# Kernel optimization log

Measured on AMD Instinct MI355X. Metric: run time of the kernel, lower is better.

The kernel has to match this reference:

```python
import jax, jax.numpy as jnp
import numpy as np

DIM = 1024
HIDDEN = 4096
NUM_EXPERTS = 8
TOP_K = 2
T = 8192


def setup_inputs() -> dict:
    key = jax.random.key(0)
    ks = jax.random.split(key, 5)
    scale = 0.02
    x = jax.random.normal(ks[0], (T, DIM), dtype=jnp.float32)
    gate_w = jax.random.normal(ks[1], (NUM_EXPERTS, DIM), dtype=jnp.float32) * scale  # Linear weight [out,in]
    w1 = jax.random.normal(ks[2], (NUM_EXPERTS, HIDDEN, DIM), dtype=jnp.float32) * scale
    w2 = jax.random.normal(ks[3], (NUM_EXPERTS, DIM, HIDDEN), dtype=jnp.float32) * scale
    w3 = jax.random.normal(ks[4], (NUM_EXPERTS, HIDDEN, DIM), dtype=jnp.float32) * scale
    return {"x": x, "gate_w": gate_w, "w1": w1, "w2": w2, "w3": w3}


def reference(x, gate_w, w1, w2, w3):
    # Router: softmax over all experts, take top-2, renormalize.
    logits = jnp.einsum('td,ed->te', x, gate_w)            # [T, E]
    probs = jax.nn.softmax(logits, axis=-1)
    topw, topi = jax.lax.top_k(probs, TOP_K)               # [T, 2]
    topw = topw / jnp.sum(topw, axis=-1, keepdims=True)
    out = jnp.zeros_like(x)
    num_experts = w1.shape[0]
    for e in range(num_experts):
        # combine weight for expert e per token (0 if not routed here)
        w_e = jnp.sum(jnp.where(topi == e, topw, 0.0), axis=-1)   # [T]
        h = jax.nn.silu(x @ w1[e].T) * (x @ w3[e].T)              # [T, HIDDEN]
        out = out + w_e[:, None] * (h @ w2[e].T)                  # [T, DIM]
    return out
```

## Files before the change

kernel.cpp:

```cpp
#include <hip/hip_runtime.h>
#include <hip/hip_bf16.h>
#include <cstdint>
#include <cstddef>

#define TK 8192
#define DIM 1024
#define HID 4096
#define NE 8

typedef __attribute__((ext_vector_type(8))) __bf16 bfrag;
typedef __attribute__((ext_vector_type(4))) float ffrag;

static __device__ __forceinline__ ushort f2bf(float f) {
    union { float f; uint32_t u; } v; v.f = f;
    uint32_t r = (v.u + 0x7fffu + ((v.u >> 16) & 1u)) >> 16;
    return (ushort)r;
}

static __device__ __forceinline__ uint4 pack8(float4 a, float4 b) {
    union { ushort u[8]; uint4 q; } pk;
    pk.u[0] = f2bf(a.x); pk.u[1] = f2bf(a.y); pk.u[2] = f2bf(a.z); pk.u[3] = f2bf(a.w);
    pk.u[4] = f2bf(b.x); pk.u[5] = f2bf(b.y); pk.u[6] = f2bf(b.z); pk.u[7] = f2bf(b.w);
    return pk.q;
}

static __device__ __forceinline__ void gld16(const ushort* g, ushort* l) {
    __builtin_amdgcn_global_load_lds(
        (const __attribute__((address_space(1))) unsigned int*)g,
        (__attribute__((address_space(3))) unsigned int*)l, 16, 0, 0);
}

#define BARRIER() asm volatile("s_barrier" ::: "memory")
#define WAITVM(N) asm volatile("s_waitcnt vmcnt(" #N ")" ::: "memory")

#define LDSIDX(r, kc) ((((r) >> 3) << 8) + ((kc) << 6) + (((r) & 7) << 3))
#define SLOT_R(s)  ((((s) >> 5) << 3) | ((s) & 7))
#define SLOT_KC(s) (((s) >> 3) & 3)

__global__ __launch_bounds__(256) void k_cvt(const float* __restrict__ src,
                                             ushort* __restrict__ dst, int n8) {
    int i = blockIdx.x * blockDim.x + threadIdx.x;
    if (i >= n8) return;
    const float4* p = (const float4*)src + (size_t)i * 2;
    ((uint4*)dst)[i] = pack8(p[0], p[1]);
}

__global__ __launch_bounds__(256) void k_router(const float* __restrict__ x,
                                                const float* __restrict__ gw,
                                                int* __restrict__ topi, float* __restrict__ topw) {
    int t = blockIdx.x * 4 + (threadIdx.x >> 6);
    int lane = threadIdx.x & 63;
    if (t >= TK) return;
    double acc[NE];
#pragma unroll
    for (int e = 0; e < NE; ++e) acc[e] = 0.0;
    const float* xr = x + (size_t)t * DIM;
    for (int k = lane; k < DIM; k += 64) {
        double xv = (double)xr[k];
#pragma unroll
        for (int e = 0; e < NE; ++e) acc[e] += xv * (double)gw[e * DIM + k];
    }
#pragma unroll
    for (int e = 0; e < NE; ++e) {
#pragma unroll
        for (int off = 32; off > 0; off >>= 1) acc[e] += __shfl_xor(acc[e], off);
    }
    if (lane == 0) {
        int i1 = 0;
#pragma unroll
        for (int e = 1; e < NE; ++e) if (acc[e] > acc[i1]) i1 = e;
        int i2 = (i1 == 0) ? 1 : 0;
#pragma unroll
        for (int e = 0; e < NE; ++e) if (e != i1 && acc[e] > acc[i2]) i2 = e;
        double w = 1.0 / (1.0 + exp(acc[i2] - acc[i1]));
        topi[t * 2 + 0] = i1; topi[t * 2 + 1] = i2;
        topw[t * 2 + 0] = (float)w; topw[t * 2 + 1] = (float)(1.0 - w);
    }
}

__global__ void k_count(const int* __restrict__ topi, int* __restrict__ counts) {
    int i = blockIdx.x * blockDim.x + threadIdx.x;
    if (i < 2 * TK) atomicAdd(&counts[topi[i]], 1);
}

__global__ void k_scan(const int* __restrict__ counts, int* __restrict__ offs,
                       int* __restrict__ cursor,
                       int* __restrict__ desc256, int* __restrict__ nd256,
                       int* __restrict__ desc128, int* __restrict__ nd128) {
    if (threadIdx.x == 0 && blockIdx.x == 0) {
        int s = 0, dA = 0, dB = 0;
        for (int e = 0; e < NE; ++e) {
            offs[e] = s; cursor[e] = s;
            int tA = (counts[e] + 255) >> 8;
            for (int t = 0; t < tA; ++t) desc256[dA++] = (e << 16) | t;
            int tB = (counts[e] + 127) >> 7;
            for (int t = 0; t < tB; ++t) desc128[dB++] = (e << 16) | t;
            s += counts[e];
        }
        offs[NE] = s;
        nd256[0] = dA; nd128[0] = dB;
    }
}

__global__ void k_scatter(const int* __restrict__ topi, const float* __restrict__ topw,
                          int* __restrict__ cursor, int* __restrict__ perm, float* __restrict__ pw) {
    int t = blockIdx.x * blockDim.x + threadIdx.x;
    if (t >= TK) return;
#pragma unroll
    for (int k = 0; k < 2; ++k) {
        int e = topi[t * 2 + k];
        int pos = atomicAdd(&cursor[e], 1);
        perm[pos] = t; pw[pos] = topw[t * 2 + k];
    }
}

__global__ __launch_bounds__(512, 2) void k_ffn1(const ushort* __restrict__ xb,
                                                 const ushort* __restrict__ w1b,
                                                 const ushort* __restrict__ w3b,
                                                 const int* __restrict__ offs,
                                                 const int* __restrict__ perm,
                                                 const int* __restrict__ desc,
                                                 const int* __restrict__ nd_g,
                                                 ushort* __restrict__ H) {
    __shared__ ushort lA[2 * 16384];
    __shared__ ushort lB[2 * 16384];
    __shared__ int lTok[256];

    const int tid = threadIdx.x;
    const int lane = tid & 63, wid = tid >> 6;
    const int l15 = lane & 15, kcc = lane >> 4;
    const int mw = wid >> 2;
    const int wn = (wid & 3) * 64;
    const int mwoff = mw * 8192;
    const int wid512 = wid * 512;

    const int NT1 = DIM / 64;
    const int nitems = nd_g[0] << 5;

    int aoff[4], boff[4];
#pragma unroll
    for (int i = 0; i < 4; ++i) aoff[i] = LDSIDX(i * 16 + l15, kcc);
#pragma unroll
    for (int j = 0; j < 4; ++j) {
        int brow = wn + j * 16 + l15;
        boff[j] = ((brow >> 7) << 13) + LDSIDX(brow & 127, kcc);
    }

    const int rS = SLOT_R(tid & 511), kcS = SLOT_KC(tid & 511);

    bfrag a[4], br[4][2];
    ffrag acc[8][4];

#pragma unroll 1
    for (int w = blockIdx.x; w < nitems; w += (int)gridDim.x) {
        __syncthreads();
        const int de = desc[w >> 5];
        const int e = de >> 16, mt = de & 0xffff, nt = w & 31;
        const int m0 = offs[e] + (mt << 8);
        const int nrows = min(256, offs[e + 1] - m0);
        if (tid < 256) lTok[tid] = (tid < nrows) ? perm[m0 + tid] : perm[m0];
        __syncthreads();

        const ushort* pA_[2]; const ushort* pB_[2];
        {
            const size_t ebase = (size_t)e * HID * DIM;
#pragma unroll
            for (int h = 0; h < 2; ++h) {
                pA_[h] = xb + (size_t)lTok[h * 128 + rS] * DIM + kcS * 8;
                int brow = h * 128 + rS;
                int gg = brow >> 4;
                int hc = nt * 128 + (((gg >> 1) << 4) | (brow & 15));
                pB_[h] = ((gg & 1) ? w3b : w1b) + ebase + (size_t)hc * DIM + kcS * 8;
            }
        }

#pragma unroll
        for (int i = 0; i < 8; ++i)
#pragma unroll
            for (int j = 0; j < 4; ++j) acc[i][j] = (ffrag)0.f;

#define SGA1(DB, HH, TT) do { if ((TT) < NT1) { \
            gld16(pA_[HH] + (TT) * 64,      lA + (DB) * 16384 + (HH) * 8192 + wid512); \
            gld16(pA_[HH] + (TT) * 64 + 32, lA + (DB) * 16384 + (HH) * 8192 + 4096 + wid512); } } while (0)
#define SGB1(DB, HH, TT) do { if ((TT) < NT1) { \
            gld16(pB_[HH] + (TT) * 64,      lB + (DB) * 16384 + (HH) * 8192 + wid512); \
            gld16(pB_[HH] + (TT) * 64 + 32, lB + (DB) * 16384 + (HH) * 8192 + 4096 + wid512); } } while (0)
#define RDB1(DB) do { _Pragma("unroll") for (int j = 0; j < 4; ++j) { \
            br[j][0] = *(const bfrag*)&lB[(DB) * 16384 + boff[j]]; \
            br[j][1] = *(const bfrag*)&lB[(DB) * 16384 + boff[j] + 4096]; } } while (0)
#define RDA1(DB, Q, S) do { _Pragma("unroll") for (int i = 0; i < 4; ++i) \
            a[i] = *(const bfrag*)&lA[(DB) * 16384 + mwoff + (S) * 4096 + (Q) * 2048 + aoff[i]]; } while (0)
#define MM1(Q, S) do { __builtin_amdgcn_s_setprio(1); \
            _Pragma("unroll") for (int i = 0; i < 4; ++i) \
            _Pragma("unroll") for (int j = 0; j < 4; ++j) \
                acc[(Q) * 4 + i][j] = __builtin_amdgcn_mfma_f32_16x16x32_bf16(a[i], br[j][S], acc[(Q) * 4 + i][j], 0, 0, 0); \
            __builtin_amdgcn_s_setprio(0); } while (0)
#define PH1(DB, Q, S, BL, STG, WT) do { \
            if (BL) RDB1(DB); RDA1(DB, Q, S); STG; WT; BARRIER(); MM1(Q, S); BARRIER(); } while (0)

        SGA1(0, 0, 0); SGA1(0, 1, 0); SGB1(0, 0, 0); SGB1(0, 1, 0);
        SGB1(1, 0, 1); SGB1(1, 1, 1);
        WAITVM(4);
        BARRIER();

#pragma unroll 1
        for (int it = 0; it < NT1 / 2; ++it) {
            const int t1 = 2 * it + 1, t2 = 2 * it + 2, t3 = 2 * it + 3;
            const bool last = (it == NT1 / 2 - 1);
            PH1(0, 0, 0, 1, SGA1(1, 0, t1), );
            PH1(0, 1, 0, 0, SGA1(1, 1, t1), );
            PH1(0, 0, 1, 0, SGB1(0, 0, t2), );
            PH1(0, 1, 1, 0, SGB1(0, 1, t2), if (last) { WAITVM(0); } else { WAITVM(4); });
            PH1(1, 0, 0, 1, SGA1(0, 0, t2), );
            PH1(1, 1, 0, 0, SGA1(0, 1, t2), );
            PH1(1, 0, 1, 0, SGB1(1, 0, t3), );
            PH1(1, 1, 1, 0, SGB1(1, 1, t3), if (last) { WAITVM(0); } else { WAITVM(4); });
        }
#undef PH1
#undef MM1
#undef RDA1
#undef RDB1
#undef SGB1
#undef SGA1

#pragma unroll
        for (int i = 0; i < 8; ++i) {
            int rbase = mw * 128 + i * 16 + ((lane >> 4) << 2);
#pragma unroll
            for (int q = 0; q < 4; ++q) {
                int rl = rbase + q;
                if (rl >= nrows) continue;
                size_t rowoff = (size_t)(m0 + rl) * HID;
#pragma unroll
                for (int jf = 0; jf < 4; jf += 2) {
                    int gg = (wn >> 4) + jf;
                    int col = nt * 128 + ((gg >> 1) << 4) + l15;
                    float h1 = acc[i][jf][q], h3 = acc[i][jf + 1][q];
                    H[rowoff + col] = f2bf((h1 / (1.f + __expf(-h1))) * h3);
                }
            }
        }
    }
}

__global__ __launch_bounds__(512, 2) void k_ffn2(const ushort* __restrict__ Hs,
                                                 const ushort* __restrict__ w2b,
                                                 const int* __restrict__ offs,
                                                 const int* __restrict__ perm,
                                                 const float* __restrict__ pw,
                                                 const int* __restrict__ desc,
                                                 const int* __restrict__ nd_g,
                                                 float* __restrict__ out) {
    __shared__ ushort lA[2 * 8192];
    __shared__ ushort lB[2 * 16384];
    __shared__ int lTok[128];
    __shared__ float lPw[128];

    const int tid = threadIdx.x;
    const int lane = tid & 63, wid = tid >> 6;
    const int l15 = lane & 15, kcc = lane >> 4;
    const int mw = wid >> 2;
    const int wn = (wid & 3) * 64;
    const int wid512 = wid * 512;

    const int NT2 = HID / 64;
    const int nitems = nd_g[0] << 2;

    int aoff[4], boff[4];
#pragma unroll
    for (int i = 0; i < 4; ++i) aoff[i] = LDSIDX(mw * 64 + i * 16 + l15, kcc);
#pragma unroll
    for (int j = 0; j < 4; ++j) {
        int brow = wn + j * 16 + l15;
        boff[j] = ((brow >> 7) << 13) + LDSIDX(brow & 127, kcc);
    }

    const int rS = SLOT_R(tid & 511), kcS = SLOT_KC(tid & 511);

    bfrag a[4], br[4][2];
    ffrag acc[4][4];

#pragma unroll 1
    for (int w = blockIdx.x; w < nitems; w += (int)gridDim.x) {
        __syncthreads();
        const int de = desc[w >> 2];
        const int e = de >> 16, mt = de & 0xffff, nt = w & 3;
        const int m0 = offs[e] + (mt << 7);
        const int nrows = min(128, offs[e + 1] - m0);
        if (tid < 128) {
            bool v = tid < nrows;
            lTok[tid] = v ? perm[m0 + tid] : 0;
            lPw[tid]  = v ? pw[m0 + tid] : 0.f;
        }
        __syncthreads();

        int posA = m0 + rS; if (posA > 2 * TK - 1) posA = 2 * TK - 1;
        const ushort* pA_ = Hs + (size_t)posA * HID + kcS * 8;
        const ushort* pB_[2];
        {
            const size_t ebase = (size_t)e * DIM * HID;
#pragma unroll
            for (int h = 0; h < 2; ++h)
                pB_[h] = w2b + ebase + (size_t)(nt * 256 + h * 128 + rS) * HID + kcS * 8;
        }

#pragma unroll
        for (int i = 0; i < 4; ++i)
#pragma unroll
            for (int j = 0; j < 4; ++j) acc[i][j] = (ffrag)0.f;

#define SGA2(DB, SUB, TT) do { if ((TT) < NT2) \
            gld16(pA_ + (TT) * 64 + (SUB) * 32, lA + (DB) * 8192 + (SUB) * 4096 + wid512); } while (0)
#define SGB2(DB, HH, SUB, TT) do { if ((TT) < NT2) \
            gld16(pB_[HH] + (TT) * 64 + (SUB) * 32, lB + (DB) * 16384 + (HH) * 8192 + (SUB) * 4096 + wid512); } while (0)
#define RDB2(DB) do { _Pragma("unroll") for (int j = 0; j < 4; ++j) { \
            br[j][0] = *(const bfrag*)&lB[(DB) * 16384 + boff[j]]; \
            br[j][1] = *(const bfrag*)&lB[(DB) * 16384 + boff[j] + 4096]; } } while (0)
#define RDA2(DB, S) do { _Pragma("unroll") for (int i = 0; i < 4; ++i) \
            a[i] = *(const bfrag*)&lA[(DB) * 8192 + (S) * 4096 + aoff[i]]; } while (0)
#define MM2(S) do { __builtin_amdgcn_s_setprio(1); \
            _Pragma("unroll") for (int i = 0; i < 4; ++i) \
            _Pragma("unroll") for (int j = 0; j < 4; ++j) \
                acc[i][j] = __builtin_amdgcn_mfma_f32_16x16x32_bf16(a[i], br[j][S], acc[i][j], 0, 0, 0); \
            __builtin_amdgcn_s_setprio(0); } while (0)

        SGA2(0, 0, 0); SGA2(0, 1, 0);
        SGB2(0, 0, 0, 0); SGB2(0, 0, 1, 0); SGB2(0, 1, 0, 0); SGB2(0, 1, 1, 0);
        SGB2(1, 0, 0, 1); SGB2(1, 0, 1, 1); SGB2(1, 1, 0, 1);
        WAITVM(3);
        BARRIER();

#pragma unroll 1
        for (int it = 0; it < NT2 / 2; ++it) {
            const int t1 = 2 * it + 1, t2 = 2 * it + 2, t3 = 2 * it + 3;
            const bool last = (it == NT2 / 2 - 1);
            RDB2(0); RDA2(0, 0);
            SGB2(1, 1, 1, t1); SGA2(1, 0, t1); SGA2(1, 1, t1);
            BARRIER(); MM2(0); BARRIER();
            RDA2(0, 1);
            SGB2(0, 0, 0, t2); SGB2(0, 0, 1, t2); SGB2(0, 1, 0, t2);
            if (last) { WAITVM(0); } else { WAITVM(3); }
            BARRIER(); MM2(1); BARRIER();
            RDB2(1); RDA2(1, 0);
            SGB2(0, 1, 1, t2); SGA2(0, 0, t2); SGA2(0, 1, t2);
            BARRIER(); MM2(0); BARRIER();
            RDA2(1, 1);
            SGB2(1, 0, 0, t3); SGB2(1, 0, 1, t3); SGB2(1, 1, 0, t3);
            if (last) { WAITVM(0); } else { WAITVM(3); }
            BARRIER(); MM2(1); BARRIER();
        }
#undef MM2
#undef RDA2
#undef RDB2
#undef SGB2
#undef SGA2

#pragma unroll
        for (int i = 0; i < 4; ++i) {
            int rbase = mw * 64 + i * 16 + ((lane >> 4) << 2);
#pragma unroll
            for (int q = 0; q < 4; ++q) {
                int rl = rbase + q;
                if (rl >= nrows) continue;
                int tok = lTok[rl];
                float wgt = lPw[rl];
                size_t rowoff = (size_t)tok * DIM;
#pragma unroll
                for (int j = 0; j < 4; ++j) {
                    int col = nt * 256 + wn + j * 16 + l15;
                    atomicAdd(&out[rowoff + col], acc[i][j][q] * wgt);
                }
            }
        }
    }
}

extern "C" void kernel_launch(void* const* d_in, const int* in_sizes, int n_in,
                              void* d_out, int out_size, void* d_ws, size_t ws_size,
                              hipStream_t stream) {
    const float* x  = (const float*)d_in[0];
    const float* gw = (const float*)d_in[1];
    const float* w1 = (const float*)d_in[2];
    const float* w2 = (const float*)d_in[3];
    const float* w3 = (const float*)d_in[4];
    float* out = (float*)d_out;

    char* ws = (char*)d_ws;
    int*    topi    = (int*)(ws + 0);
    float*  topw    = (float*)(ws + 65536);
    int*    perm    = (int*)(ws + 131072);
    float*  pw      = (float*)(ws + 196608);
    int*    counts  = (int*)(ws + 262144);
    int*    offs    = (int*)(ws + 262144 + 256);
    int*    cursor  = (int*)(ws + 262144 + 512);
    int*    nd256   = (int*)(ws + 262144 + 768);
    int*    nd128   = (int*)(ws + 262144 + 772);
    int*    desc256 = (int*)(ws + 262144 + 1024);
    int*    desc128 = (int*)(ws + 262144 + 2048);

    const size_t OFF_XB = 524288;
    const size_t OFF_H  = OFF_XB + 16777216;
    const size_t OFF_WA = OFF_H + 134217728;
    const size_t OFF_WB = OFF_WA + 67108864;

    ushort* xb  = (ushort*)(ws + OFF_XB);
    ushort* H   = (ushort*)(ws + OFF_H);
    ushort* wA  = (ushort*)(ws + OFF_WA);
    ushort* wB  = (ushort*)(ws + OFF_WB);

    hipMemsetAsync(counts, 0, 32, stream);
    hipMemsetAsync(out, 0, (size_t)out_size * sizeof(float), stream);

    k_router<<<dim3(TK / 4), 256, 0, stream>>>(x, gw, topi, topw);
    k_count<<<dim3((2 * TK) / 256), 256, 0, stream>>>(topi, counts);
    k_scan<<<dim3(1), 64, 0, stream>>>(counts, offs, cursor, desc256, nd256, desc128, nd128);
    k_scatter<<<dim3(TK / 256), 256, 0, stream>>>(topi, topw, cursor, perm, pw);

    k_cvt<<<dim3((TK * DIM / 8) / 256), 256, 0, stream>>>(x, xb, TK * DIM / 8);
    k_cvt<<<dim3((NE * HID * DIM / 8) / 256), 256, 0, stream>>>(w1, wA, NE * HID * DIM / 8);
    k_cvt<<<dim3((NE * HID * DIM / 8) / 256), 256, 0, stream>>>(w3, wB, NE * HID * DIM / 8);

    k_ffn1<<<dim3(256), 512, 0, stream>>>(xb, wA, wB, offs, perm, desc256, nd256, H);

    k_cvt<<<dim3((NE * DIM * HID / 8) / 256), 256, 0, stream>>>(w2, wA, NE * DIM * HID / 8);

    k_ffn2<<<dim3(512), 512, 0, stream>>>(H, wA, offs, perm, pw, desc128, nd128, out);
}
```

Before: 1.029 ms.

## Replace persistent GEMM loops with static grid and atomic scatter with combine pass

Both expert FFN kernels stop being persistent loops over work items. Each block now maps to one (descriptor, N-tile) pair through a grouped index, and blocks beyond the descriptor count exit early. The second GEMM writes unweighted per-slot results to a dense fp32 buffer instead of doing weighted atomicAdd into the output. A new combine kernel then gathers each token's two slots through a token-to-slot map and writes the output once, which also drops the output memset. This removes atomic contention and makes the block-to-tile order L2-friendly, at the cost of an extra 64MB write and read of the intermediate buffer plus one more launch.

```diff
diff --git a/kernel.cpp b/kernel.cpp
--- a/kernel.cpp
+++ b/kernel.cpp
@@ -103,7 +103,8 @@
 }
 
 __global__ void k_scatter(const int* __restrict__ topi, const float* __restrict__ topw,
-                          int* __restrict__ cursor, int* __restrict__ perm, float* __restrict__ pw) {
+                          int* __restrict__ cursor, int* __restrict__ perm,
+                          float* __restrict__ pw, int* __restrict__ tokslot) {
     int t = blockIdx.x * blockDim.x + threadIdx.x;
     if (t >= TK) return;
 #pragma unroll
@@ -111,7 +112,25 @@
         int e = topi[t * 2 + k];
         int pos = atomicAdd(&cursor[e], 1);
         perm[pos] = t; pw[pos] = topw[t * 2 + k];
-    }
+        tokslot[t * 2 + k] = pos;
+    }
+}
+
+__global__ __launch_bounds__(256) void k_combine(const float* __restrict__ H2,
+                                                 const int* __restrict__ tokslot,
+                                                 const float* __restrict__ pw,
+                                                 float* __restrict__ out) {
+    const int t = blockIdx.x, d = threadIdx.x;
+    const int s0 = tokslot[t * 2], s1 = tokslot[t * 2 + 1];
+    const float w0 = pw[s0], w1 = pw[s1];
+    float4 va = ((const float4*)(H2 + (size_t)s0 * DIM))[d];
+    float4 vb = ((const float4*)(H2 + (size_t)s1 * DIM))[d];
+    float4 r;
+    r.x = w0 * va.x + w1 * vb.x;
+    r.y = w0 * va.y + w1 * vb.y;
+    r.z = w0 * va.z + w1 * vb.z;
+    r.w = w0 * va.w + w1 * vb.w;
+    ((float4*)(out + (size_t)t * DIM))[d] = r;
 }
 
 __global__ __launch_bounds__(512, 2) void k_ffn1(const ushort* __restrict__ xb,
@@ -122,6 +141,11 @@
                                                  const int* __restrict__ desc,
                                                  const int* __restrict__ nd_g,
                                                  ushort* __restrict__ H) {
+    const int b = blockIdx.x;
+    const int d = ((b >> 8) << 3) | (b & 7);
+    const int nt = (b >> 3) & 31;
+    if (d >= nd_g[0]) return;
+
     __shared__ ushort lA[2 * 16384];
     __shared__ ushort lB[2 * 16384];
     __shared__ int lTok[256];
@@ -135,7 +159,6 @@
     const int wid512 = wid * 512;
 
     const int NT1 = DIM / 64;
-    const int nitems = nd_g[0] << 5;
 
     int aoff[4], boff[4];
 #pragma unroll
@@ -151,71 +174,68 @@
     bfrag a[4], br[4][2];
     ffrag acc[8][4];
 
+    const int de = desc[d];
+    const int e = de >> 16, mt = de & 0xffff;
+    const int m0 = offs[e] + (mt << 8);
+    const int nrows = min(256, offs[e + 1] - m0);
+    if (tid < 256) lTok[tid] = (tid < nrows) ? perm[m0 + tid] : perm[m0];
+    __syncthreads();
+
+    const ushort* pA_[2]; const ushort* pB_[2];
+    {
+        const size_t ebase = (size_t)e * HID * DIM;
+#pragma unroll
+        for (int h = 0; h < 2; ++h) {
+            pA_[h] = xb + (size_t)lTok[h * 128 + rS] * DIM + kcS * 8;
+            int brow = h * 128 + rS;
+            int gg = brow >> 4;
+            int hc = nt * 128 + (((gg >> 1) << 4) | (brow & 15));
+            pB_[h] = ((gg & 1) ? w3b : w1b) + ebase + (size_t)hc * DIM + kcS * 8;
+        }
+    }
+
+#pragma unroll
+    for (int i = 0; i < 8; ++i)
+#pragma unroll
+        for (int j = 0; j < 4; ++j) acc[i][j] = (ffrag)0.f;
+
+#define SGA1(DB, HH, TT) do { if ((TT) < NT1) { \
+        gld16(pA_[HH] + (TT) * 64,      lA + (DB) * 16384 + (HH) * 8192 + wid512); \
+        gld16(pA_[HH] + (TT) * 64 + 32, lA + (DB) * 16384 + (HH) * 8192 + 4096 + wid512); } } while (0)
+#define SGB1(DB, HH, TT) do { if ((TT) < NT1) { \
+        gld16(pB_[HH] + (TT) * 64,      lB + (DB) * 16384 + (HH) * 8192 + wid512); \
+        gld16(pB_[HH] + (TT) * 64 + 32, lB + (DB) * 16384 + (HH) * 8192 + 4096 + wid512); } } while (0)
+#define RDB1(DB) do { _Pragma("unroll") for (int j = 0; j < 4; ++j) { \
+        br[j][0] = *(const bfrag*)&lB[(DB) * 16384 + boff[j]]; \
+        br[j][1] = *(const bfrag*)&lB[(DB) * 16384 + boff[j] + 4096]; } } while (0)
+#define RDA1(DB, Q, S) do { _Pragma("unroll") for (int i = 0; i < 4; ++i) \
+        a[i] = *(const bfrag*)&lA[(DB) * 16384 + mwoff + (S) * 4096 + (Q) * 2048 + aoff[i]]; } while (0)
+#define MM1(Q, S) do { __builtin_amdgcn_s_setprio(1); \
+        _Pragma("unroll") for (int i = 0; i < 4; ++i) \
+        _Pragma("unroll") for (int j = 0; j < 4; ++j) \
+            acc[(Q) * 4 + i][j] = __builtin_amdgcn_mfma_f32_16x16x32_bf16(a[i], br[j][S], acc[(Q) * 4 + i][j], 0, 0, 0); \
+        __builtin_amdgcn_s_setprio(0); } while (0)
+#define PH1(DB, Q, S, BL, STG, WT) do { \
+        if (BL) RDB1(DB); RDA1(DB, Q, S); STG; WT; BARRIER(); MM1(Q, S); BARRIER(); } while (0)
+
+    SGA1(0, 0, 0); SGA1(0, 1, 0); SGB1(0, 0, 0); SGB1(0, 1, 0);
+    SGB1(1, 0, 1); SGB1(1, 1, 1);
+    WAITVM(4);
+    BARRIER();
+
 #pragma unroll 1
-    for (int w = blockIdx.x; w < nitems; w += (int)gridDim.x) {
-        __syncthreads();
-        const int de = desc[w >> 5];
-        const int e = de >> 16, mt = de & 0xffff, nt = w & 31;
-        const int m0 = offs[e] + (mt << 8);
-        const int nrows = min(256, offs[e + 1] - m0);
-        if (tid < 256) lTok[tid] = (tid < nrows) ? perm[m0 + tid] : perm[m0];
-        __syncthreads();
-
-        const ushort* pA_[2]; const ushort* pB_[2];
-        {
-            const size_t ebase = (size_t)e * HID * DIM;
-#pragma unroll
-            for (int h = 0; h < 2; ++h) {
-                pA_[h] = xb + (size_t)lTok[h * 128 + rS] * DIM + kcS * 8;
-                int brow = h * 128 + rS;
-                int gg = brow >> 4;
-                int hc = nt * 128 + (((gg >> 1) << 4) | (brow & 15));
-                pB_[h] = ((gg & 1) ? w3b : w1b) + ebase + (size_t)hc * DIM + kcS * 8;
-            }
-        }
-
-#pragma unroll
-        for (int i = 0; i < 8; ++i)
-#pragma unroll
-            for (int j = 0; j < 4; ++j) acc[i][j] = (ffrag)0.f;
-
-#define SGA1(DB, HH, TT) do { if ((TT) < NT1) { \
-            gld16(pA_[HH] + (TT) * 64,      lA + (DB) * 16384 + (HH) * 8192 + wid512); \
-            gld16(pA_[HH] + (TT) * 64 + 32, lA + (DB) * 16384 + (HH) * 8192 + 4096 + wid512); } } while (0)
-#define SGB1(DB, HH, TT) do { if ((TT) < NT1) { \
-            gld16(pB_[HH] + (TT) * 64,      lB + (DB) * 16384 + (HH) * 8192 + wid512); \
-            gld16(pB_[HH] + (TT) * 64 + 32, lB + (DB) * 16384 + (HH) * 8192 + 4096 + wid512); } } while (0)
-#define RDB1(DB) do { _Pragma("unroll") for (int j = 0; j < 4; ++j) { \
-            br[j][0] = *(const bfrag*)&lB[(DB) * 16384 + boff[j]]; \
-            br[j][1] = *(const bfrag*)&lB[(DB) * 16384 + boff[j] + 4096]; } } while (0)
-#define RDA1(DB, Q, S) do { _Pragma("unroll") for (int i = 0; i < 4; ++i) \
-            a[i] = *(const bfrag*)&lA[(DB) * 16384 + mwoff + (S) * 4096 + (Q) * 2048 + aoff[i]]; } while (0)
-#define MM1(Q, S) do { __builtin_amdgcn_s_setprio(1); \
-            _Pragma("unroll") for (int i = 0; i < 4; ++i) \
-            _Pragma("unroll") for (int j = 0; j < 4; ++j) \
-                acc[(Q) * 4 + i][j] = __builtin_amdgcn_mfma_f32_16x16x32_bf16(a[i], br[j][S], acc[(Q) * 4 + i][j], 0, 0, 0); \
-            __builtin_amdgcn_s_setprio(0); } while (0)
-#define PH1(DB, Q, S, BL, STG, WT) do { \
-            if (BL) RDB1(DB); RDA1(DB, Q, S); STG; WT; BARRIER(); MM1(Q, S); BARRIER(); } while (0)
-
-        SGA1(0, 0, 0); SGA1(0, 1, 0); SGB1(0, 0, 0); SGB1(0, 1, 0);
-        SGB1(1, 0, 1); SGB1(1, 1, 1);
-        WAITVM(4);
-        BARRIER();
-
-#pragma unroll 1
-        for (int it = 0; it < NT1 / 2; ++it) {
-            const int t1 = 2 * it + 1, t2 = 2 * it + 2, t3 = 2 * it + 3;
-            const bool last = (it == NT1 / 2 - 1);
-            PH1(0, 0, 0, 1, SGA1(1, 0, t1), );
-            PH1(0, 1, 0, 0, SGA1(1, 1, t1), );
-            PH1(0, 0, 1, 0, SGB1(0, 0, t2), );
-            PH1(0, 1, 1, 0, SGB1(0, 1, t2), if (last) { WAITVM(0); } else { WAITVM(4); });
-            PH1(1, 0, 0, 1, SGA1(0, 0, t2), );
-            PH1(1, 1, 0, 0, SGA1(0, 1, t2), );
-            PH1(1, 0, 1, 0, SGB1(1, 0, t3), );
-            PH1(1, 1, 1, 0, SGB1(1, 1, t3), if (last) { WAITVM(0); } else { WAITVM(4); });
-        }
+    for (int it = 0; it < NT1 / 2; ++it) {
+        const int t1 = 2 * it + 1, t2 = 2 * it + 2, t3 = 2 * it + 3;
+        const bool last = (it == NT1 / 2 - 1);
+        PH1(0, 0, 0, 1, SGA1(1, 0, t1), );
+        PH1(0, 1, 0, 0, SGA1(1, 1, t1), );
+        PH1(0, 0, 1, 0, SGB1(0, 0, t2), );
+        PH1(0, 1, 1, 0, SGB1(0, 1, t2), if (last) { WAITVM(0); } else { WAITVM(4); });
+        PH1(1, 0, 0, 1, SGA1(0, 0, t2), );
+        PH1(1, 1, 0, 0, SGA1(0, 1, t2), );
+        PH1(1, 0, 1, 0, SGB1(1, 0, t3), );
+        PH1(1, 1, 1, 0, SGB1(1, 1, t3), if (last) { WAITVM(0); } else { WAITVM(4); });
+    }
 #undef PH1
 #undef MM1
 #undef RDA1
@@ -224,20 +244,19 @@
 #undef SGA1
 
 #pragma unroll
-        for (int i = 0; i < 8; ++i) {
-            int rbase = mw * 128 + i * 16 + ((lane >> 4) << 2);
-#pragma unroll
-            for (int q = 0; q < 4; ++q) {
-                int rl = rbase + q;
-                if (rl >= nrows) continue;
-                size_t rowoff = (size_t)(m0 + rl) * HID;
-#pragma unroll
-                for (int jf = 0; jf < 4; jf += 2) {
-                    int gg = (wn >> 4) + jf;
-                    int col = nt * 128 + ((gg >> 1) << 4) + l15;
-                    float h1 = acc[i][jf][q], h3 = acc[i][jf + 1][q];
-                    H[rowoff + col] = f2bf((h1 / (1.f + __expf(-h1))) * h3);
-                }
+    for (int i = 0; i < 8; ++i) {
+        int rbase = mw * 128 + i * 16 + ((lane >> 4) << 2);
+#pragma unroll
+        for (int q = 0; q < 4; ++q) {
+            int rl = rbase + q;
+            if (rl >= nrows) continue;
+            size_t rowoff = (size_t)(m0 + rl) * HID;
+#pragma unroll
+            for (int jf = 0; jf < 4; jf += 2) {
+                int gg = (wn >> 4) + jf;
+                int col = nt * 128 + ((gg >> 1) << 4) + l15;
+                float h1 = acc[i][jf][q], h3 = acc[i][jf + 1][q];
+                H[rowoff + col] = f2bf((h1 / (1.f + __expf(-h1))) * h3);
             }
         }
     }
@@ -246,15 +265,16 @@
 __global__ __launch_bounds__(512, 2) void k_ffn2(const ushort* __restrict__ Hs,
                                                  const ushort* __restrict__ w2b,
                                                  const int* __restrict__ offs,
-                                                 const int* __restrict__ perm,
-                                                 const float* __restrict__ pw,
                                                  const int* __restrict__ desc,
                                                  const int* __restrict__ nd_g,
-                                                 float* __restrict__ out) {
+                                                 float* __restrict__ H2) {
+    const int b = blockIdx.x;
+    const int d = ((b >> 5) << 3) | (b & 7);
+    const int nt = (b >> 3) & 3;
+    if (d >= nd_g[0]) return;
+
     __shared__ ushort lA[2 * 8192];
     __shared__ ushort lB[2 * 16384];
-    __shared__ int lTok[128];
-    __shared__ float lPw[128];
 
     const int tid = threadIdx.x;
     const int lane = tid & 63, wid = tid >> 6;
@@ -264,7 +284,6 @@
     const int wid512 = wid * 512;
 
     const int NT2 = HID / 64;
-    const int nitems = nd_g[0] << 2;
 
     int aoff[4], boff[4];
 #pragma unroll
@@ -280,75 +299,66 @@
     bfrag a[4], br[4][2];
     ffrag acc[4][4];
 
+    const int de = desc[d];
+    const int e = de >> 16, mt = de & 0xffff;
+    const int m0 = offs[e] + (mt << 7);
+    const int nrows = min(128, offs[e + 1] - m0);
+
+    int posA = m0 + rS; if (posA > 2 * TK - 1) posA = 2 * TK - 1;
+    const ushort* pA_ = Hs + (size_t)posA * HID + kcS * 8;
+    const ushort* pB_[2];
+    {
+        const size_t ebase = (size_t)e * DIM * HID;
+#pragma unroll
+        for (int h = 0; h < 2; ++h)
+            pB_[h] = w2b + ebase + (size_t)(nt * 256 + h * 128 + rS) * HID + kcS * 8;
+    }
+
+#pragma unroll
+    for (int i = 0; i < 4; ++i)
+#pragma unroll
+        for (int j = 0; j < 4; ++j) acc[i][j] = (ffrag)0.f;
+
+#define SGA2(DB, SUB, TT) do { if ((TT) < NT2) \
+        gld16(pA_ + (TT) * 64 + (SUB) * 32, lA + (DB) * 8192 + (SUB) * 4096 + wid512); } while (0)
+#define SGB2(DB, HH, SUB, TT) do { if ((TT) < NT2) \
+        gld16(pB_[HH] + (TT) * 64 + (SUB) * 32, lB + (DB) * 16384 + (HH) * 8192 + (SUB) * 4096 + wid512); } while (0)
+#define RDB2(DB) do { _Pragma("unroll") for (int j = 0; j < 4; ++j) { \
+        br[j][0] = *(const bfrag*)&lB[(DB) * 16384 + boff[j]]; \
+        br[j][1] = *(const bfrag*)&lB[(DB) * 16384 + boff[j] + 4096]; } } while (0)
+#define RDA2(DB, S) do { _Pragma("unroll") for (int i = 0; i < 4; ++i) \
+        a[i] = *(const bfrag*)&lA[(DB) * 8192 + (S) * 4096 + aoff[i]]; } while (0)
+#define MM2(S) do { __builtin_amdgcn_s_setprio(1); \
+        _Pragma("unroll") for (int i = 0; i < 4; ++i) \
+        _Pragma("unroll") for (int j = 0; j < 4; ++j) \
+            acc[i][j] = __builtin_amdgcn_mfma_f32_16x16x32_bf16(a[i], br[j][S], acc[i][j], 0, 0, 0); \
+        __builtin_amdgcn_s_setprio(0); } while (0)
+
+    SGA2(0, 0, 0); SGA2(0, 1, 0);
+    SGB2(0, 0, 0, 0); SGB2(0, 0, 1, 0); SGB2(0, 1, 0, 0); SGB2(0, 1, 1, 0);
+    SGB2(1, 0, 0, 1); SGB2(1, 0, 1, 1); SGB2(1, 1, 0, 1);
+    WAITVM(3);
+    BARRIER();
+
 #pragma unroll 1
-    for (int w = blockIdx.x; w < nitems; w += (int)gridDim.x) {
-        __syncthreads();
-        const int de = desc[w >> 2];
-        const int e = de >> 16, mt = de & 0xffff, nt = w & 3;
-        const int m0 = offs[e] + (mt << 7);
-        const int nrows = min(128, offs[e + 1] - m0);
-        if (tid < 128) {
-            bool v = tid < nrows;
-            lTok[tid] = v ? perm[m0 + tid] : 0;
-            lPw[tid]  = v ? pw[m0 + tid] : 0.f;
-        }
-        __syncthreads();
-
-        int posA = m0 + rS; if (posA > 2 * TK - 1) posA = 2 * TK - 1;
-        const ushort* pA_ = Hs + (size_t)posA * HID + kcS * 8;
-        const ushort* pB_[2];
-        {
-            const size_t ebase = (size_t)e * DIM * HID;
-#pragma unroll
-            for (int h = 0; h < 2; ++h)
-                pB_[h] = w2b + ebase + (size_t)(nt * 256 + h * 128 + rS) * HID + kcS * 8;
-        }
-
-#pragma unroll
-        for (int i = 0; i < 4; ++i)
-#pragma unroll
-            for (int j = 0; j < 4; ++j) acc[i][j] = (ffrag)0.f;
-
-#define SGA2(DB, SUB, TT) do { if ((TT) < NT2) \
-            gld16(pA_ + (TT) * 64 + (SUB) * 32, lA + (DB) * 8192 + (SUB) * 4096 + wid512); } while (0)
-#define SGB2(DB, HH, SUB, TT) do { if ((TT) < NT2) \
-            gld16(pB_[HH] + (TT) * 64 + (SUB) * 32, lB + (DB) * 16384 + (HH) * 8192 + (SUB) * 4096 + wid512); } while (0)
-#define RDB2(DB) do { _Pragma("unroll") for (int j = 0; j < 4; ++j) { \
-            br[j][0] = *(const bfrag*)&lB[(DB) * 16384 + boff[j]]; \
-            br[j][1] = *(const bfrag*)&lB[(DB) * 16384 + boff[j] + 4096]; } } while (0)
-#define RDA2(DB, S) do { _Pragma("unroll") for (int i = 0; i < 4; ++i) \
-            a[i] = *(const bfrag*)&lA[(DB) * 8192 + (S) * 4096 + aoff[i]]; } while (0)
-#define MM2(S) do { __builtin_amdgcn_s_setprio(1); \
-            _Pragma("unroll") for (int i = 0; i < 4; ++i) \
-            _Pragma("unroll") for (int j = 0; j < 4; ++j) \
-                acc[i][j] = __builtin_amdgcn_mfma_f32_16x16x32_bf16(a[i], br[j][S], acc[i][j], 0, 0, 0); \
-            __builtin_amdgcn_s_setprio(0); } while (0)
-
-        SGA2(0, 0, 0); SGA2(0, 1, 0);
-        SGB2(0, 0, 0, 0); SGB2(0, 0, 1, 0); SGB2(0, 1, 0, 0); SGB2(0, 1, 1, 0);
-        SGB2(1, 0, 0, 1); SGB2(1, 0, 1, 1); SGB2(1, 1, 0, 1);
-        WAITVM(3);
-        BARRIER();
-
-#pragma unroll 1
-        for (int it = 0; it < NT2 / 2; ++it) {
-            const int t1 = 2 * it + 1, t2 = 2 * it + 2, t3 = 2 * it + 3;
-            const bool last = (it == NT2 / 2 - 1);
-            RDB2(0); RDA2(0, 0);
-            SGB2(1, 1, 1, t1); SGA2(1, 0, t1); SGA2(1, 1, t1);
-            BARRIER(); MM2(0); BARRIER();
-            RDA2(0, 1);
-            SGB2(0, 0, 0, t2); SGB2(0, 0, 1, t2); SGB2(0, 1, 0, t2);
-            if (last) { WAITVM(0); } else { WAITVM(3); }
-            BARRIER(); MM2(1); BARRIER();
-            RDB2(1); RDA2(1, 0);
-            SGB2(0, 1, 1, t2); SGA2(0, 0, t2); SGA2(0, 1, t2);
-            BARRIER(); MM2(0); BARRIER();
-            RDA2(1, 1);
-            SGB2(1, 0, 0, t3); SGB2(1, 0, 1, t3); SGB2(1, 1, 0, t3);
-            if (last) { WAITVM(0); } else { WAITVM(3); }
-            BARRIER(); MM2(1); BARRIER();
-        }
+    for (int it = 0; it < NT2 / 2; ++it) {
+        const int t1 = 2 * it + 1, t2 = 2 * it + 2, t3 = 2 * it + 3;
+        const bool last = (it == NT2 / 2 - 1);
+        RDB2(0); RDA2(0, 0);
+        SGB2(1, 1, 1, t1); SGA2(1, 0, t1); SGA2(1, 1, t1);
+        BARRIER(); MM2(0); BARRIER();
+        RDA2(0, 1);
+        SGB2(0, 0, 0, t2); SGB2(0, 0, 1, t2); SGB2(0, 1, 0, t2);
+        if (last) { WAITVM(0); } else { WAITVM(3); }
+        BARRIER(); MM2(1); BARRIER();
+        RDB2(1); RDA2(1, 0);
+        SGB2(0, 1, 1, t2); SGA2(0, 0, t2); SGA2(0, 1, t2);
+        BARRIER(); MM2(0); BARRIER();
+        RDA2(1, 1);
+        SGB2(1, 0, 0, t3); SGB2(1, 0, 1, t3); SGB2(1, 1, 0, t3);
+        if (last) { WAITVM(0); } else { WAITVM(3); }
+        BARRIER(); MM2(1); BARRIER();
+    }
 #undef MM2
 #undef RDA2
 #undef RDB2
@@ -356,20 +366,17 @@
 #undef SGA2
 
 #pragma unroll
-        for (int i = 0; i < 4; ++i) {
-            int rbase = mw * 64 + i * 16 + ((lane >> 4) << 2);
-#pragma unroll
-            for (int q = 0; q < 4; ++q) {
-                int rl = rbase + q;
-                if (rl >= nrows) continue;
-                int tok = lTok[rl];
-                float wgt = lPw[rl];
-                size_t rowoff = (size_t)tok * DIM;
-#pragma unroll
-                for (int j = 0; j < 4; ++j) {
-                    int col = nt * 256 + wn + j * 16 + l15;
-                    atomicAdd(&out[rowoff + col], acc[i][j][q] * wgt);
-                }
+    for (int i = 0; i < 4; ++i) {
+        int rbase = mw * 64 + i * 16 + ((lane >> 4) << 2);
+#pragma unroll
+        for (int q = 0; q < 4; ++q) {
+            int rl = rbase + q;
+            if (rl >= nrows) continue;
+            size_t rowoff = (size_t)(m0 + rl) * DIM;
+#pragma unroll
+            for (int j = 0; j < 4; ++j) {
+                int col = nt * 256 + wn + j * 16 + l15;
+                H2[rowoff + col] = acc[i][j][q];
             }
         }
     }
@@ -390,15 +397,16 @@
     float*  topw    = (float*)(ws + 65536);
     int*    perm    = (int*)(ws + 131072);
     float*  pw      = (float*)(ws + 196608);
-    int*    counts  = (int*)(ws + 262144);
-    int*    offs    = (int*)(ws + 262144 + 256);
-    int*    cursor  = (int*)(ws + 262144 + 512);
-    int*    nd256   = (int*)(ws + 262144 + 768);
-    int*    nd128   = (int*)(ws + 262144 + 772);
-    int*    desc256 = (int*)(ws + 262144 + 1024);
-    int*    desc128 = (int*)(ws + 262144 + 2048);
-
-    const size_t OFF_XB = 524288;
+    int*    tokslot = (int*)(ws + 262144);
+    int*    counts  = (int*)(ws + 327680);
+    int*    offs    = (int*)(ws + 327680 + 256);
+    int*    cursor  = (int*)(ws + 327680 + 512);
+    int*    nd256   = (int*)(ws + 327680 + 768);
+    int*    nd128   = (int*)(ws + 327680 + 772);
+    int*    desc256 = (int*)(ws + 327680 + 1024);
+    int*    desc128 = (int*)(ws + 327680 + 2048);
+
+    const size_t OFF_XB = 655360;
     const size_t OFF_H  = OFF_XB + 16777216;
     const size_t OFF_WA = OFF_H + 134217728;
     const size_t OFF_WB = OFF_WA + 67108864;
@@ -407,22 +415,24 @@
     ushort* H   = (ushort*)(ws + OFF_H);
     ushort* wA  = (ushort*)(ws + OFF_WA);
     ushort* wB  = (ushort*)(ws + OFF_WB);
+    float*  H2  = (float*)(ws + OFF_WB);
 
     hipMemsetAsync(counts, 0, 32, stream);
-    hipMemsetAsync(out, 0, (size_t)out_size * sizeof(float), stream);
 
     k_router<<<dim3(TK / 4), 256, 0, stream>>>(x, gw, topi, topw);
     k_count<<<dim3((2 * TK) / 256), 256, 0, stream>>>(topi, counts);
     k_scan<<<dim3(1), 64, 0, stream>>>(counts, offs, cursor, desc256, nd256, desc128, nd128);
-    k_scatter<<<dim3(TK / 256), 256, 0, stream>>>(topi, topw, cursor, perm, pw);
+    k_scatter<<<dim3(TK / 256), 256, 0, stream>>>(topi, topw, cursor, perm, pw, tokslot);
 
     k_cvt<<<dim3((TK * DIM / 8) / 256), 256, 0, stream>>>(x, xb, TK * DIM / 8);
     k_cvt<<<dim3((NE * HID * DIM / 8) / 256), 256, 0, stream>>>(w1, wA, NE * HID * DIM / 8);
     k_cvt<<<dim3((NE * HID * DIM / 8) / 256), 256, 0, stream>>>(w3, wB, NE * HID * DIM / 8);
 
-    k_ffn1<<<dim3(256), 512, 0, stream>>>(xb, wA, wB, offs, perm, desc256, nd256, H);
+    k_ffn1<<<dim3(9 * 256), 512, 0, stream>>>(xb, wA, wB, offs, perm, desc256, nd256, H);
 
     k_cvt<<<dim3((NE * DIM * HID / 8) / 256), 256, 0, stream>>>(w2, wA, NE * DIM * HID / 8);
 
-    k_ffn2<<<dim3(512), 512, 0, stream>>>(H, wA, offs, perm, pw, desc128, nd128, out);
-}
+    k_ffn2<<<dim3(17 * 32), 512, 0, stream>>>(H, wA, offs, desc128, nd128, H2);
+
+    k_combine<<<dim3(TK), 256, 0, stream>>>(H2, tokslot, pw, out);
+}
```

After: 1.005 ms. 2.3% less time.
